# Kernel optimization log

Hardware: AMD Instinct MI355X
Metric: run time of the kernel (lower is better)

Reference implementation:

```python
import jax, jax.numpy as jnp
import numpy as np

B, Q, K, C, H = 4, 1024, 1024, 1024, 16
L = C            # latent_dim (== in_dim per module construction)
CH = L // H      # head_dim = 64


def _ln(x, w, b):
    m = jnp.mean(x, -1, keepdims=True)
    v = jnp.mean((x - m) ** 2, -1, keepdims=True)
    return (x - m) * jax.lax.rsqrt(v + 1e-5) * w + b


def setup_inputs() -> dict:
    key = jax.random.key(0)
    ks = jax.random.split(key, 16)
    s = 0.02
    return {
        "queries": jax.random.normal(ks[0], (B, Q, C), jnp.float32),
        "contexts": jax.random.normal(ks[1], (B, K, C), jnp.float32),
        "queries_hidden": jax.random.normal(ks[2], (B, Q, L), jnp.float32),
        "sa_norm_w": jnp.ones((C,), jnp.float32),
        "sa_norm_b": jnp.zeros((C,), jnp.float32),
        "sa_qkv_w": jax.random.normal(ks[3], (C, 2 * L + C), jnp.float32) * s,
        "sa_out_w": jax.random.normal(ks[4], (C, C), jnp.float32) * s,
        "sa_out_b": jnp.zeros((C,), jnp.float32),
        "ca_norm_w": jnp.ones((C,), jnp.float32),
        "ca_norm_b": jnp.zeros((C,), jnp.float32),
        "gru_w_ih": jax.random.normal(ks[5], (3 * L, C), jnp.float32) * s,
        "gru_w_hh": jax.random.normal(ks[6], (3 * L, L), jnp.float32) * s,
        "gru_b_ih": jnp.zeros((3 * L,), jnp.float32),
        "gru_b_hh": jnp.zeros((3 * L,), jnp.float32),
        "ca_k_w": jax.random.normal(ks[7], (C, L), jnp.float32) * s,
        "ca_v_w": jax.random.normal(ks[8], (C, C), jnp.float32) * s,
        "ca_out_w": jax.random.normal(ks[9], (C, C), jnp.float32) * s,
        "ca_out_b": jnp.zeros((C,), jnp.float32),
        "ln1_w": jnp.ones((C,), jnp.float32),
        "ln1_b": jnp.zeros((C,), jnp.float32),
        "lin1_w": jax.random.normal(ks[10], (C, 2 * C), jnp.float32) * s,
        "ln2_w": jnp.ones((2 * C,), jnp.float32),
        "ln2_b": jnp.zeros((2 * C,), jnp.float32),
        "lin2_w": jax.random.normal(ks[11], (2 * C, C), jnp.float32) * s,
    }


def reference(queries, contexts, queries_hidden,
              sa_norm_w, sa_norm_b, sa_qkv_w, sa_out_w, sa_out_b,
              ca_norm_w, ca_norm_b, gru_w_ih, gru_w_hh, gru_b_ih, gru_b_hh,
              ca_k_w, ca_v_w, ca_out_w, ca_out_b,
              ln1_w, ln1_b, lin1_w, ln2_w, ln2_b, lin2_w):
    scale = 1.0 / jnp.sqrt(jnp.asarray(C, queries.dtype))

    # ---- SelfAttention (pre-norm, residual) ----
    xn = _ln(queries, sa_norm_w, sa_norm_b)
    qkv = (xn @ sa_qkv_w).reshape(B, Q, H, -1)          # [B,Q,H, 2*CH + C/H]
    q, k, v = jnp.split(qkv, [CH, 2 * CH], axis=-1)
    e = jnp.einsum('nqhc,nkhc->nhqk', q, k) * scale
    a = jax.nn.softmax(e, axis=-1)
    o = jnp.einsum('nhqk,nkhc->nqhc', a, v).reshape(B, Q, C)
    x = o @ sa_out_w + sa_out_b + queries

    # ---- AttentionDynamicQuery (GRU-updated queries, cross-attn) ----
    x_pre = x
    xn = _ln(x, ca_norm_w, ca_norm_b)
    xf = xn.reshape(B * Q, C)
    hf = queries_hidden.reshape(B * Q, L)
    gi = xf @ gru_w_ih.T + gru_b_ih                     # [BQ, 3L]
    gh = hf @ gru_w_hh.T + gru_b_hh
    gir, giz, gin = jnp.split(gi, 3, axis=-1)
    ghr, ghz, ghn = jnp.split(gh, 3, axis=-1)
    r = jax.nn.sigmoid(gir + ghr)
    z = jax.nn.sigmoid(giz + ghz)
    n = jnp.tanh(gin + r * ghn)
    h = (1.0 - z) * n + z * hf                          # PyTorch GRUCell update
    qh = h.reshape(B, Q, H, CH)                         # new queries_hidden

    kk = (contexts @ ca_k_w).reshape(B, K, H, CH)
    vv = (contexts @ ca_v_w).reshape(B, K, H, C // H)
    energy = jnp.einsum('nqhc,nkhc->nhqk', qh, kk)      # returned UNscaled
    att = jax.nn.softmax(energy * scale, axis=-1)
    o = jnp.einsum('nhqk,nkhc->nqhc', att, vv).reshape(B, Q, C)
    x = o @ ca_out_w + ca_out_b + x_pre

    # ---- MLP: LN -> SiLU -> Linear -> LN -> SiLU -> Linear, residual ----
    m = jax.nn.silu(_ln(x, ln1_w, ln1_b)) @ lin1_w
    m = jax.nn.silu(_ln(m, ln2_w, ln2_b)) @ lin2_w
    out = x + m                                         # dropout(p=0) = identity
    return (out, energy, qh)
```

## Files before the change

kernel.cpp:

```cpp
#include <hip/hip_runtime.h>
#include <hip/hip_bf16.h>
#include <math.h>

static constexpr float SCALE = 0.03125f;

typedef __attribute__((ext_vector_type(4))) float f32x4;
typedef __attribute__((ext_vector_type(8))) __bf16 bf16x8;
typedef __attribute__((ext_vector_type(4))) __bf16 bf16x4;

__device__ __forceinline__ void g2l16(const void* g, void* l) {
  __builtin_amdgcn_global_load_lds(
      (const __attribute__((address_space(1))) unsigned int*)g,
      (__attribute__((address_space(3))) unsigned int*)l,
      16, 0, 0);
}

__global__ __launch_bounds__(256) void prep_all(
    const float* __restrict__ sa_qkv_w, const float* __restrict__ ca_k_w,
    const float* __restrict__ ca_v_w, const float* __restrict__ sa_out_w,
    const float* __restrict__ ca_out_w, const float* __restrict__ lin1_w,
    const float* __restrict__ lin2_w, const float* __restrict__ gru_w_ih,
    const float* __restrict__ gru_w_hh, const float* __restrict__ qhid,
    const float* __restrict__ contexts,
    __bf16* __restrict__ qkvT, __bf16* __restrict__ kT, __bf16* __restrict__ vT,
    __bf16* __restrict__ saoT, __bf16* __restrict__ caoT, __bf16* __restrict__ lin1T,
    __bf16* __restrict__ lin2T, __bf16* __restrict__ ihB, __bf16* __restrict__ hhB,
    __bf16* __restrict__ qhB, __bf16* __restrict__ ctxB) {
  int bid = blockIdx.x;
  int t = threadIdx.x;
  if (bid >= 2816) {
    const float* csrc; __bf16* cdst; int cbase;
    if (bid < 4352)      { csrc = gru_w_ih; cdst = ihB;  cbase = 2816; }
    else if (bid < 5888) { csrc = gru_w_hh; cdst = hhB;  cbase = 4352; }
    else if (bid < 7936) { csrc = qhid;     cdst = qhB;  cbase = 5888; }
    else                 { csrc = contexts; cdst = ctxB; cbase = 7936; }
    size_t idx = ((size_t)(bid - cbase) * 256 + t) * 8;
    float4 a = *(const float4*)(csrc + idx);
    float4 b = *(const float4*)(csrc + idx + 4);
    bf16x8 o = {(__bf16)a.x,(__bf16)a.y,(__bf16)a.z,(__bf16)a.w,
                (__bf16)b.x,(__bf16)b.y,(__bf16)b.z,(__bf16)b.w};
    *(bf16x8*)(cdst + idx) = o;
    return;
  }
  const float* src; __bf16* dst; int Kd, N, base;
  if (bid < 768)       { src = sa_qkv_w; dst = qkvT;  Kd = 1024; N = 3072; base = 0; }
  else if (bid < 1024) { src = ca_k_w;   dst = kT;    Kd = 1024; N = 1024; base = 768; }
  else if (bid < 1280) { src = ca_v_w;   dst = vT;    Kd = 1024; N = 1024; base = 1024; }
  else if (bid < 1536) { src = sa_out_w; dst = saoT;  Kd = 1024; N = 1024; base = 1280; }
  else if (bid < 1792) { src = ca_out_w; dst = caoT;  Kd = 1024; N = 1024; base = 1536; }
  else if (bid < 2304) { src = lin1_w;   dst = lin1T; Kd = 1024; N = 2048; base = 1792; }
  else                 { src = lin2_w;   dst = lin2T; Kd = 2048; N = 1024; base = 2304; }
  int tid = bid - base;
  int ntx = N >> 6;
  int n0 = (tid % ntx) * 64, k0 = (tid / ntx) * 64;
  __shared__ float tile[64][65];
  #pragma unroll
  for (int i = 0; i < 16; ++i) {
    int idx = i * 256 + t; int r = idx >> 6, c = idx & 63;
    tile[r][c] = src[(size_t)(k0 + r) * N + n0 + c];
  }
  __syncthreads();
  #pragma unroll
  for (int i = 0; i < 16; ++i) {
    int idx = i * 256 + t; int r = idx >> 6, c = idx & 63;
    dst[(size_t)(n0 + r) * Kd + k0 + c] = (__bf16)tile[c][r];
  }
}

template <int NV>
__global__ __launch_bounds__(256) void ln_bf16(
    const float* __restrict__ xf, const __bf16* __restrict__ xb,
    const float* __restrict__ w, const float* __restrict__ b,
    __bf16* __restrict__ out, int silu) {
  const int D = NV * 1024;
  int row = blockIdx.x, t = threadIdx.x;
  float vals[NV * 4];
  float s = 0.f, s2 = 0.f;
  #pragma unroll
  for (int i = 0; i < NV; ++i) {
    int c = (i * 256 + t) * 4;
    float4 v;
    if (xf) {
      v = *(const float4*)(xf + (size_t)row * D + c);
    } else {
      bf16x4 vb = *(const bf16x4*)(xb + (size_t)row * D + c);
      v = make_float4((float)vb[0], (float)vb[1], (float)vb[2], (float)vb[3]);
    }
    vals[i*4+0] = v.x; vals[i*4+1] = v.y; vals[i*4+2] = v.z; vals[i*4+3] = v.w;
    s += v.x + v.y + v.z + v.w;
    s2 += v.x*v.x + v.y*v.y + v.z*v.z + v.w*v.w;
  }
  #pragma unroll
  for (int off = 32; off > 0; off >>= 1) {
    s += __shfl_xor(s, off);
    s2 += __shfl_xor(s2, off);
  }
  __shared__ float red[4], red2[4];
  int wv = t >> 6;
  if ((t & 63) == 0) { red[wv] = s; red2[wv] = s2; }
  __syncthreads();
  float S  = red[0] + red[1] + red[2] + red[3];
  float S2 = red2[0] + red2[1] + red2[2] + red2[3];
  float mean = S / D;
  float var = S2 / D - mean * mean;
  float rs = rsqrtf(var + 1e-5f);
  #pragma unroll
  for (int i = 0; i < NV; ++i) {
    int c = (i * 256 + t) * 4;
    bf16x4 o;
    #pragma unroll
    for (int j = 0; j < 4; ++j) {
      float v = (vals[i*4+j] - mean) * rs * w[c+j] + b[c+j];
      if (silu) v = v / (1.f + __expf(-v));
      o[j] = (__bf16)v;
    }
    *(bf16x4*)(out + (size_t)row * D + c) = o;
  }
}

__device__ __forceinline__ void gemm_body(
    const __bf16* __restrict__ A, long long lda,
    const __bf16* __restrict__ B, long long ldb,
    float* __restrict__ outF, __bf16* __restrict__ outB, long long ldc,
    const float* __restrict__ bias, const float* __restrict__ res,
    int K, int bm, int bn) {
  __shared__ __bf16 Asm0[8192];
  __shared__ __bf16 Bsm0[8192];
  __shared__ __bf16 Asm1[8192];
  __shared__ __bf16 Bsm1[8192];
  int t = threadIdx.x;
  int lane = t & 63, w = t >> 6;
  int l15 = lane & 15, kg = lane >> 4;
  int wm = (w >> 1) * 64, wn = (w & 1) * 64;

  f32x4 acc[4][4];
  #pragma unroll
  for (int i = 0; i < 4; ++i)
    #pragma unroll
    for (int j = 0; j < 4; ++j) acc[i][j] = (f32x4)(0.0f);

  const __bf16* ga[4]; const __bf16* gb[4];
  int lo[4];
  #pragma unroll
  for (int i = 0; i < 4; ++i) {
    int slot = i * 256 + t;
    int row = slot >> 3, s = slot & 7;
    int sx = s ^ (row & 7);
    ga[i] = A + (size_t)(bm + row) * lda + (sx << 3);
    gb[i] = B + (size_t)(bn + row) * ldb + (sx << 3);
    lo[i] = (i * 256 + w * 64) << 3;
  }

  auto STAGE = [&](__bf16* As, __bf16* Bs, int k0) {
    #pragma unroll
    for (int i = 0; i < 4; ++i) g2l16(ga[i] + k0, As + lo[i]);
    #pragma unroll
    for (int i = 0; i < 4; ++i) g2l16(gb[i] + k0, Bs + lo[i]);
  };
  auto COMPUTE = [&](const __bf16* As, const __bf16* Bs) {
    #pragma unroll
    for (int kk = 0; kk < 2; ++kk) {
      bf16x8 af[4], bfr[4];
      #pragma unroll
      for (int mi = 0; mi < 4; ++mi) {
        int row = wm + mi * 16 + l15;
        int ks = kk * 4 + kg;
        af[mi] = *(const bf16x8*)(As + row * 64 + ((ks ^ (row & 7)) << 3));
      }
      #pragma unroll
      for (int ni = 0; ni < 4; ++ni) {
        int row = wn + ni * 16 + l15;
        int ks = kk * 4 + kg;
        bfr[ni] = *(const bf16x8*)(Bs + row * 64 + ((ks ^ (row & 7)) << 3));
      }
      #pragma unroll
      for (int mi = 0; mi < 4; ++mi)
        #pragma unroll
        for (int ni = 0; ni < 4; ++ni)
          acc[mi][ni] = __builtin_amdgcn_mfma_f32_16x16x32_bf16(
              af[mi], bfr[ni], acc[mi][ni], 0, 0, 0);
    }
  };
  #define GEMM_SYNC() do { \
    asm volatile("s_waitcnt vmcnt(0)" ::: "memory"); \
    __builtin_amdgcn_s_barrier(); \
    __builtin_amdgcn_sched_barrier(0); \
  } while (0)

  STAGE(Asm0, Bsm0, 0);
  GEMM_SYNC();
  int nk = K >> 6;
  for (int kt = 0; kt + 2 < nk; kt += 2) {
    STAGE(Asm1, Bsm1, (kt + 1) << 6);
    COMPUTE(Asm0, Bsm0);
    GEMM_SYNC();
    STAGE(Asm0, Bsm0, (kt + 2) << 6);
    COMPUTE(Asm1, Bsm1);
    GEMM_SYNC();
  }
  STAGE(Asm1, Bsm1, (nk - 1) << 6);
  COMPUTE(Asm0, Bsm0);
  GEMM_SYNC();
  COMPUTE(Asm1, Bsm1);
  #undef GEMM_SYNC

  #pragma unroll
  for (int mi = 0; mi < 4; ++mi) {
    #pragma unroll
    for (int ni = 0; ni < 4; ++ni) {
      int rbase = bm + wm + mi * 16 + kg * 4;
      int c = bn + wn + ni * 16 + l15;
      #pragma unroll
      for (int r = 0; r < 4; ++r) {
        float val = acc[mi][ni][r];
        if (bias) val += bias[c];
        size_t off = (size_t)(rbase + r) * ldc + c;
        if (res) val += res[off];
        if (outF) outF[off] = val;
        if (outB) outB[off] = (__bf16)val;
      }
    }
  }
}

__global__ __launch_bounds__(256) void gemm_bf16(
    const __bf16* __restrict__ A, long long lda,
    const __bf16* __restrict__ B, long long ldb,
    float* __restrict__ outF, __bf16* __restrict__ outB, long long ldc,
    const float* __restrict__ bias, const float* __restrict__ res, int K) {
  int nwg = gridDim.x * gridDim.y;
  int orig = blockIdx.y * gridDim.x + blockIdx.x;
  int swz = (orig & 7) * (nwg >> 3) + (orig >> 3);
  gemm_body(A, lda, B, ldb, outF, outB, ldc, bias, res, K,
            (swz / gridDim.x) * 128, (swz % gridDim.x) * 128);
}

__global__ __launch_bounds__(256) void gemm_dual(
    const __bf16* __restrict__ A0, long long lda0, const __bf16* __restrict__ B0, long long ldb0,
    float* __restrict__ oF0, __bf16* __restrict__ oB0, long long ldc0,
    const float* __restrict__ bias0, const float* __restrict__ res0, int K0, int gx0, int nb0,
    const __bf16* __restrict__ A1, long long lda1, const __bf16* __restrict__ B1, long long ldb1,
    float* __restrict__ oF1, __bf16* __restrict__ oB1, long long ldc1,
    const float* __restrict__ bias1, const float* __restrict__ res1, int K1, int gx1) {
  int bid = blockIdx.x;
  if (bid < nb0) {
    int swz = (bid & 7) * (nb0 >> 3) + (bid >> 3);
    gemm_body(A0, lda0, B0, ldb0, oF0, oB0, ldc0, bias0, res0, K0,
              (swz / gx0) * 128, (swz % gx0) * 128);
  } else {
    int b = bid - nb0;
    int nb1 = gridDim.x - nb0;
    int swz = (b & 7) * (nb1 >> 3) + (b >> 3);
    gemm_body(A1, lda1, B1, ldb1, oF1, oB1, ldc1, bias1, res1, K1,
              (swz / gx1) * 128, (swz % gx1) * 128);
  }
}

__global__ __launch_bounds__(256) void vtrans(
    const __bf16* __restrict__ V, long long v_sb, long long v_sh, int v_sm,
    __bf16* __restrict__ VT) {
  __shared__ __bf16 tile[64][72];
  int g = blockIdx.y, b = g >> 4, h = g & 15;
  int k0 = blockIdx.x * 64;
  const __bf16* Vb = V + (size_t)b * v_sb + (size_t)h * v_sh;
  int t = threadIdx.x;
  #pragma unroll
  for (int i = 0; i < 2; ++i) {
    int idx = i * 256 + t;
    int k = idx >> 3, dc = (idx & 7) * 8;
    bf16x8 v = *(const bf16x8*)(Vb + (size_t)(k0 + k) * v_sm + dc);
    #pragma unroll
    for (int j = 0; j < 8; ++j) tile[dc + j][k] = v[j];
  }
  __syncthreads();
  #pragma unroll
  for (int i = 0; i < 2; ++i) {
    int idx = i * 256 + t;
    int d = idx >> 3, kc = (idx & 7) * 8;
    bf16x8 v;
    #pragma unroll
    for (int j = 0; j < 8; ++j) v[j] = tile[d][kc + j];
    *(bf16x8*)(VT + ((size_t)g * 64 + d) * 1024 + k0 + kc) = v;
  }
}

template <int E>
__global__ __launch_bounds__(256) void flash_attn(
    const __bf16* __restrict__ Qb, long long q_sb, long long q_sh, int q_sm,
    const __bf16* __restrict__ Kb, long long k_sb, long long k_sh, int k_sm,
    const __bf16* __restrict__ VT, __bf16* __restrict__ Ob,
    float* __restrict__ energyOut, float scale) {
  __shared__ __bf16 Ksm[3][4096];
  __shared__ __bf16 Vsm[3][4096];
  __shared__ __bf16 Psm[128 * 64];
  __shared__ float corr_l[128];
  __shared__ float l_l[128];
  int g = blockIdx.y, b = g >> 4, h = g & 15;
  int qt = blockIdx.x * 128;
  const __bf16* Qg = Qb + (size_t)b * q_sb + (size_t)h * q_sh;
  const __bf16* Kg = Kb + (size_t)b * k_sb + (size_t)h * k_sh;
  const __bf16* Vg = VT + (size_t)g * 65536;
  int t = threadIdx.x, lane = t & 63, w = t >> 6;
  int l15 = lane & 15, kg = lane >> 4;
  int wq = w * 32;

  bf16x8 qf[2][2];
  #pragma unroll
  for (int nq = 0; nq < 2; ++nq)
    #pragma unroll
    for (int kk = 0; kk < 2; ++kk)
      qf[nq][kk] = *(const bf16x8*)(
          Qg + (size_t)(qt + wq + nq * 16 + l15) * q_sm + kk * 32 + kg * 8);

  f32x4 acc_o[2][4];
  #pragma unroll
  for (int i = 0; i < 2; ++i)
    #pragma unroll
    for (int j = 0; j < 4; ++j) acc_o[i][j] = (f32x4)(0.0f);
  float m_run[2] = {-1e30f, -1e30f};
  float l_run[2] = {0.f, 0.f};

  const __bf16* gK[2]; const __bf16* gV[2];
  int lo[2];
  #pragma unroll
  for (int i = 0; i < 2; ++i) {
    int slot = i * 256 + t;
    int row = slot >> 3, s = slot & 7, sx = s ^ (row & 7);
    gK[i] = Kg + (size_t)row * k_sm + (sx << 3);
    gV[i] = Vg + (size_t)row * 1024 + (sx << 3);
    lo[i] = (i * 256 + w * 64) << 3;
  }

  #pragma unroll
  for (int i = 0; i < 2; ++i) g2l16(gK[i], &Ksm[0][lo[i]]);
  #pragma unroll
  for (int i = 0; i < 2; ++i) g2l16(gV[i], &Vsm[0][lo[i]]);
  #pragma unroll
  for (int i = 0; i < 2; ++i) g2l16(gK[i] + (size_t)64 * k_sm, &Ksm[1][lo[i]]);
  #pragma unroll
  for (int i = 0; i < 2; ++i) g2l16(gV[i] + 64, &Vsm[1][lo[i]]);

  int rb = 0;
  for (int kvt = 0; kvt < 16; ++kvt) {
    if (E) {
      if (kvt == 0)       asm volatile("s_waitcnt vmcnt(4)" ::: "memory");
      else if (kvt == 1)  asm volatile("s_waitcnt vmcnt(12)" ::: "memory");
      else if (kvt == 15) asm volatile("s_waitcnt vmcnt(16)" ::: "memory");
      else                asm volatile("s_waitcnt vmcnt(20)" ::: "memory");
    } else {
      if (kvt == 15)      asm volatile("s_waitcnt vmcnt(0)" ::: "memory");
      else                asm volatile("s_waitcnt vmcnt(4)" ::: "memory");
    }
    __builtin_amdgcn_s_barrier();
    __builtin_amdgcn_sched_barrier(0);

    if (kvt < 14) {
      int sbuf = rb >= 1 ? rb - 1 : rb + 2;
      size_t ko = (size_t)(kvt + 2) << 6;
      #pragma unroll
      for (int i = 0; i < 2; ++i) g2l16(gK[i] + ko * k_sm, &Ksm[sbuf][lo[i]]);
      #pragma unroll
      for (int i = 0; i < 2; ++i) g2l16(gV[i] + ko, &Vsm[sbuf][lo[i]]);
    }
    const __bf16* Ks = Ksm[rb];
    const __bf16* Vs = Vsm[rb];

    f32x4 accs[4][2];
    #pragma unroll
    for (int i = 0; i < 4; ++i)
      #pragma unroll
      for (int j = 0; j < 2; ++j) accs[i][j] = (f32x4)(0.0f);
    __builtin_amdgcn_s_setprio(1);
    #pragma unroll
    for (int tt = 0; tt < 4; ++tt) {
      bf16x8 kf[2];
      #pragma unroll
      for (int kk = 0; kk < 2; ++kk) {
        int row = tt * 16 + l15;
        int ks = kk * 4 + kg;
        kf[kk] = *(const bf16x8*)(Ks + row * 64 + ((ks ^ (row & 7)) << 3));
      }
      #pragma unroll
      for (int nq = 0; nq < 2; ++nq)
        #pragma unroll
        for (int kk = 0; kk < 2; ++kk)
          accs[tt][nq] = __builtin_amdgcn_mfma_f32_16x16x32_bf16(
              kf[kk], qf[nq][kk], accs[tt][nq], 0, 0, 0);
    }
    __builtin_amdgcn_s_setprio(0);

    if (E) {
      int kv0 = kvt << 6;
      float* eg = energyOut + ((size_t)g << 20);
      #pragma unroll
      for (int nq = 0; nq < 2; ++nq) {
        int q = qt + wq + nq * 16 + l15;
        #pragma unroll
        for (int tt = 0; tt < 4; ++tt)
          __builtin_nontemporal_store(
              accs[tt][nq], (f32x4*)(eg + (size_t)q * 1024 + kv0 + tt * 16 + kg * 4));
      }
    }

    #pragma unroll
    for (int nq = 0; nq < 2; ++nq) {
      float tmax = -1e30f;
      #pragma unroll
      for (int tt = 0; tt < 4; ++tt)
        #pragma unroll
        for (int r = 0; r < 4; ++r) tmax = fmaxf(tmax, accs[tt][nq][r]);
      tmax *= scale;
      tmax = fmaxf(tmax, __shfl_xor(tmax, 16));
      tmax = fmaxf(tmax, __shfl_xor(tmax, 32));
      float m_new = fmaxf(m_run[nq], tmax);
      float corr = __expf(m_run[nq] - m_new);
      m_run[nq] = m_new;
      int q = wq + nq * 16 + l15;
      float psum = 0.f;
      #pragma unroll
      for (int tt = 0; tt < 4; ++tt) {
        bf16x4 p4;
        #pragma unroll
        for (int r = 0; r < 4; ++r) {
          float p = __expf(accs[tt][nq][r] * scale - m_new);
          psum += p;
          p4[r] = (__bf16)p;
        }
        int kvs = (tt * 16 + kg * 4) ^ ((q & 7) << 3);
        *(bf16x4*)(Psm + q * 64 + kvs) = p4;
      }
      psum += __shfl_xor(psum, 16);
      psum += __shfl_xor(psum, 32);
      l_run[nq] = l_run[nq] * corr + psum;
      if (kg == 0) corr_l[q] = corr;
    }

    #pragma unroll
    for (int mq = 0; mq < 2; ++mq) {
      f32x4 c4 = *(const f32x4*)&corr_l[wq + mq * 16 + kg * 4];
      #pragma unroll
      for (int nd = 0; nd < 4; ++nd)
        #pragma unroll
        for (int r = 0; r < 4; ++r) acc_o[mq][nd][r] *= c4[r];
    }
    __builtin_amdgcn_s_setprio(1);
    #pragma unroll
    for (int kk = 0; kk < 2; ++kk) {
      bf16x8 pf[2], vf[4];
      #pragma unroll
      for (int mq = 0; mq < 2; ++mq) {
        int row = wq + mq * 16 + l15;
        int kvs = (kk * 32 + kg * 8) ^ ((row & 7) << 3);
        pf[mq] = *(const bf16x8*)(Psm + row * 64 + kvs);
      }
      #pragma unroll
      for (int nd = 0; nd < 4; ++nd) {
        int vrow = nd * 16 + l15;
        vf[nd] = *(const bf16x8*)(Vs + vrow * 64 + (((kk * 4 + kg) ^ (vrow & 7)) << 3));
      }
      #pragma unroll
      for (int mq = 0; mq < 2; ++mq)
        #pragma unroll
        for (int nd = 0; nd < 4; ++nd)
          acc_o[mq][nd] = __builtin_amdgcn_mfma_f32_16x16x32_bf16(
              pf[mq], vf[nd], acc_o[mq][nd], 0, 0, 0);
    }
    __builtin_amdgcn_s_setprio(0);
    rb = rb == 2 ? 0 : rb + 1;
  }

  #pragma unroll
  for (int nq = 0; nq < 2; ++nq)
    if (kg == 0) l_l[wq + nq * 16 + l15] = l_run[nq];
  __syncthreads();

  #pragma unroll
  for (int mq = 0; mq < 2; ++mq) {
    f32x4 lv = *(const f32x4*)&l_l[wq + mq * 16 + kg * 4];
    #pragma unroll
    for (int nd = 0; nd < 4; ++nd) {
      int col = h * 64 + nd * 16 + l15;
      #pragma unroll
      for (int r = 0; r < 4; ++r) {
        int qrow = qt + wq + mq * 16 + kg * 4 + r;
        Ob[(size_t)(b * 1024 + qrow) * 1024 + col] = (__bf16)(acc_o[mq][nd][r] / lv[r]);
      }
    }
  }
}

__global__ __launch_bounds__(256) void gru_kernel(
    const __bf16* __restrict__ gi, const __bf16* __restrict__ gh,
    const float* __restrict__ hf, float* __restrict__ qh, __bf16* __restrict__ qhb) {
  size_t e0 = ((size_t)blockIdx.x * 256 + threadIdx.x) * 8;
  int row = (int)(e0 >> 10), col = (int)(e0 & 1023);
  size_t base = (size_t)row * 3072 + col;
  bf16x8 vir = *(const bf16x8*)(gi + base);
  bf16x8 viz = *(const bf16x8*)(gi + base + 1024);
  bf16x8 vin = *(const bf16x8*)(gi + base + 2048);
  bf16x8 vhr = *(const bf16x8*)(gh + base);
  bf16x8 vhz = *(const bf16x8*)(gh + base + 1024);
  bf16x8 vhn = *(const bf16x8*)(gh + base + 2048);
  float4 h0 = *(const float4*)(hf + e0);
  float4 h1 = *(const float4*)(hf + e0 + 4);
  float hv[8] = {h0.x, h0.y, h0.z, h0.w, h1.x, h1.y, h1.z, h1.w};
  float q[8];
  #pragma unroll
  for (int j = 0; j < 8; ++j) {
    float r = 1.f / (1.f + __expf(-((float)vir[j] + (float)vhr[j])));
    float z = 1.f / (1.f + __expf(-((float)viz[j] + (float)vhz[j])));
    float n = tanhf((float)vin[j] + r * (float)vhn[j]);
    q[j] = (1.f - z) * n + z * hv[j];
  }
  *(float4*)(qh + e0)     = make_float4(q[0], q[1], q[2], q[3]);
  *(float4*)(qh + e0 + 4) = make_float4(q[4], q[5], q[6], q[7]);
  bf16x8 qb;
  #pragma unroll
  for (int j = 0; j < 8; ++j) qb[j] = (__bf16)q[j];
  *(bf16x8*)(qhb + e0) = qb;
}

extern "C" void kernel_launch(void* const* d_in, const int* in_sizes, int n_in,
                              void* d_out, int out_size, void* d_ws, size_t ws_size,
                              hipStream_t stream) {
  (void)in_sizes; (void)n_in; (void)out_size; (void)ws_size;
  const float* queries   = (const float*)d_in[0];
  const float* contexts  = (const float*)d_in[1];
  const float* qhid      = (const float*)d_in[2];
  const float* sa_norm_w = (const float*)d_in[3];
  const float* sa_norm_b = (const float*)d_in[4];
  const float* sa_qkv_w  = (const float*)d_in[5];
  const float* sa_out_w  = (const float*)d_in[6];
  const float* sa_out_b  = (const float*)d_in[7];
  const float* ca_norm_w = (const float*)d_in[8];
  const float* ca_norm_b = (const float*)d_in[9];
  const float* gru_w_ih  = (const float*)d_in[10];
  const float* gru_w_hh  = (const float*)d_in[11];
  const float* gru_b_ih  = (const float*)d_in[12];
  const float* gru_b_hh  = (const float*)d_in[13];
  const float* ca_k_w    = (const float*)d_in[14];
  const float* ca_v_w    = (const float*)d_in[15];
  const float* ca_out_w  = (const float*)d_in[16];
  const float* ca_out_b  = (const float*)d_in[17];
  const float* ln1_w     = (const float*)d_in[18];
  const float* ln1_b     = (const float*)d_in[19];
  const float* lin1_w    = (const float*)d_in[20];
  const float* ln2_w     = (const float*)d_in[21];
  const float* ln2_b     = (const float*)d_in[22];
  const float* lin2_w    = (const float*)d_in[23];

  float* out0   = (float*)d_out;
  float* energy = out0 + (size_t)4194304;
  float* qh_out = out0 + (size_t)71303168;

  const size_t MM = 1u << 20;
  float* ws = (float*)d_ws;
  float*  X     = ws;
  float*  X2    = ws + 4 * MM;
  __bf16* M1B    = (__bf16*)(ws + 9 * MM);
  __bf16* XN_b   = (__bf16*)(ws + 17 * MM);
  __bf16* QHID_b = (__bf16*)(ws + 19 * MM);
  __bf16* CTX_b  = (__bf16*)(ws + 21 * MM);
  __bf16* O_b    = (__bf16*)(ws + 23 * MM);
  __bf16* VT_b   = (__bf16*)(ws + 25 * MM);
  __bf16* QKV_b  = (__bf16*)(ws + 27 * MM);
  __bf16* KV_b   = (__bf16*)(ws + 27 * MM);
  __bf16* LN2_b  = (__bf16*)(ws);
  __bf16* qkvT   = (__bf16*)(ws + 33 * MM);
  __bf16* ihB    = (__bf16*)(ws + 34 * MM + MM / 2);
  __bf16* hhB    = (__bf16*)(ws + 36 * MM);
  __bf16* kT     = (__bf16*)(ws + 37 * MM + MM / 2);
  __bf16* vT     = (__bf16*)(ws + 38 * MM);
  __bf16* saoT   = (__bf16*)(ws + 38 * MM + MM / 2);
  __bf16* caoT   = (__bf16*)(ws + 39 * MM);
  __bf16* lin1T  = (__bf16*)(ws + 39 * MM + MM / 2);
  __bf16* lin2T  = (__bf16*)(ws + 40 * MM + MM / 2);
  __bf16* GI_b = (__bf16*)energy;
  __bf16* GH_b = (__bf16*)(energy + 6 * MM);

  const long long QKV_SB = 1024LL * 3072;
  const long long KV_SB  = 1024LL * 2048;

  prep_all<<<9984, 256, 0, stream>>>(
      sa_qkv_w, ca_k_w, ca_v_w, sa_out_w, ca_out_w, lin1_w, lin2_w,
      gru_w_ih, gru_w_hh, qhid, contexts,
      qkvT, kT, vT, saoT, caoT, lin1T, lin2T, ihB, hhB, QHID_b, CTX_b);

  ln_bf16<1><<<4096, 256, 0, stream>>>(queries, nullptr, sa_norm_w, sa_norm_b, XN_b, 0);
  gemm_bf16<<<dim3(24, 32), 256, 0, stream>>>(
      XN_b, 1024, qkvT, 1024, nullptr, QKV_b, 3072, nullptr, nullptr, 1024);
  vtrans<<<dim3(16, 64), 256, 0, stream>>>(QKV_b + 128, QKV_SB, 192, 3072, VT_b);
  flash_attn<0><<<dim3(8, 64), 256, 0, stream>>>(
      QKV_b, QKV_SB, 192, 3072, QKV_b + 64, QKV_SB, 192, 3072,
      VT_b, O_b, nullptr, SCALE);
  gemm_dual<<<1024, 256, 0, stream>>>(
      O_b, 1024, saoT, 1024, X, nullptr, 1024, sa_out_b, queries, 1024, 8, 256,
      QHID_b, 1024, hhB, 1024, nullptr, GH_b, 3072, gru_b_hh, nullptr, 1024, 24);

  ln_bf16<1><<<4096, 256, 0, stream>>>(X, nullptr, ca_norm_w, ca_norm_b, XN_b, 0);
  gemm_dual<<<1280, 256, 0, stream>>>(
      XN_b, 1024, ihB, 1024, nullptr, GI_b, 3072, gru_b_ih, nullptr, 1024, 24, 768,
      CTX_b, 1024, kT, 1024, nullptr, KV_b, 2048, nullptr, nullptr, 1024, 16);
  gru_kernel<<<2048, 256, 0, stream>>>(GI_b, GH_b, qhid, qh_out, QHID_b );

  vtrans<<<dim3(16, 64), 256, 0, stream>>>(KV_b + 1024, KV_SB, 64, 2048, VT_b);
  flash_attn<1><<<dim3(8, 64), 256, 0, stream>>>(
      QHID_b, 1024LL * 1024, 64, 1024, KV_b, KV_SB, 64, 2048,
      VT_b, O_b, energy, SCALE);
  gemm_bf16<<<dim3(8, 32), 256, 0, stream>>>(
      O_b, 1024, caoT, 1024, X2, nullptr, 1024, ca_out_b, X, 1024);

  ln_bf16<1><<<4096, 256, 0, stream>>>(X2, nullptr, ln1_w, ln1_b, XN_b, 1);
  gemm_bf16<<<dim3(16, 32), 256, 0, stream>>>(
      XN_b, 1024, lin1T, 1024, nullptr, M1B, 2048, nullptr, nullptr, 1024);
  ln_bf16<2><<<4096, 256, 0, stream>>>(nullptr, M1B, ln2_w, ln2_b, LN2_b, 1);
  gemm_bf16<<<dim3(8, 32), 256, 0, stream>>>(
      LN2_b, 2048, lin2T, 2048, out0, nullptr, 1024, nullptr, X2, 2048);
}
```

Before: 621.7 us.

## Fuse first LayerNorm into prep and compute cross-attn V transposed directly

Folds the self-attention LayerNorm into the prep kernel as extra blocks, which removes one launch. The cross-attention V projection is now computed directly in transposed form, as vT times contexts per batch, inside the QKV gemm_dual launch. This drops the separate vtrans pass for cross-attention and shrinks the later K/V gemm to K only. It relies on vT being the transposed weight laid out so the product gives the VT layout that flash_attn expects, and on the batch offset of 1<<20 elements being correct.

```diff
diff --git a/kernel.cpp b/kernel.cpp
--- a/kernel.cpp
+++ b/kernel.cpp
@@ -22,12 +22,42 @@
     const float* __restrict__ lin2_w, const float* __restrict__ gru_w_ih,
     const float* __restrict__ gru_w_hh, const float* __restrict__ qhid,
     const float* __restrict__ contexts,
+    const float* __restrict__ queries, const float* __restrict__ sa_norm_w,
+    const float* __restrict__ sa_norm_b,
     __bf16* __restrict__ qkvT, __bf16* __restrict__ kT, __bf16* __restrict__ vT,
     __bf16* __restrict__ saoT, __bf16* __restrict__ caoT, __bf16* __restrict__ lin1T,
     __bf16* __restrict__ lin2T, __bf16* __restrict__ ihB, __bf16* __restrict__ hhB,
-    __bf16* __restrict__ qhB, __bf16* __restrict__ ctxB) {
+    __bf16* __restrict__ qhB, __bf16* __restrict__ ctxB, __bf16* __restrict__ xnB) {
   int bid = blockIdx.x;
   int t = threadIdx.x;
+  if (bid >= 9984) {
+    int row = bid - 9984;
+    int c = t * 4;
+    float4 v = *(const float4*)(queries + (size_t)row * 1024 + c);
+    float s = v.x + v.y + v.z + v.w;
+    float s2 = v.x*v.x + v.y*v.y + v.z*v.z + v.w*v.w;
+    #pragma unroll
+    for (int off = 32; off > 0; off >>= 1) {
+      s += __shfl_xor(s, off);
+      s2 += __shfl_xor(s2, off);
+    }
+    __shared__ float red[4], red2[4];
+    int wv = t >> 6;
+    if ((t & 63) == 0) { red[wv] = s; red2[wv] = s2; }
+    __syncthreads();
+    float S  = red[0] + red[1] + red[2] + red[3];
+    float S2 = red2[0] + red2[1] + red2[2] + red2[3];
+    float mean = S / 1024.f;
+    float var = S2 / 1024.f - mean * mean;
+    float rs = rsqrtf(var + 1e-5f);
+    float vv[4] = {v.x, v.y, v.z, v.w};
+    bf16x4 o;
+    #pragma unroll
+    for (int j = 0; j < 4; ++j)
+      o[j] = (__bf16)((vv[j] - mean) * rs * sa_norm_w[c+j] + sa_norm_b[c+j]);
+    *(bf16x4*)(xnB + (size_t)row * 1024 + c) = o;
+    return;
+  }
   if (bid >= 2816) {
     const float* csrc; __bf16* cdst; int cbase;
     if (bid < 4352)      { csrc = gru_w_ih; cdst = ihB;  cbase = 2816; }
@@ -241,7 +271,8 @@
     const float* __restrict__ bias0, const float* __restrict__ res0, int K0, int gx0, int nb0,
     const __bf16* __restrict__ A1, long long lda1, const __bf16* __restrict__ B1, long long ldb1,
     float* __restrict__ oF1, __bf16* __restrict__ oB1, long long ldc1,
-    const float* __restrict__ bias1, const float* __restrict__ res1, int K1, int gx1) {
+    const float* __restrict__ bias1, const float* __restrict__ res1, int K1, int gx1,
+    int batchB1) {
   int bid = blockIdx.x;
   if (bid < nb0) {
     int swz = (bid & 7) * (nb0 >> 3) + (bid >> 3);
@@ -251,8 +282,16 @@
     int b = bid - nb0;
     int nb1 = gridDim.x - nb0;
     int swz = (b & 7) * (nb1 >> 3) + (b >> 3);
-    gemm_body(A1, lda1, B1, ldb1, oF1, oB1, ldc1, bias1, res1, K1,
-              (swz / gx1) * 128, (swz % gx1) * 128);
+    int tm = swz / gx1, bn = (swz % gx1) * 128;
+    if (batchB1) {
+      int batch = tm >> 3;
+      gemm_body(A1, lda1, B1 + ((size_t)batch << 20), ldb1, nullptr,
+                oB1 + ((size_t)batch << 20), ldc1, bias1, res1, K1,
+                (tm & 7) * 128, bn);
+    } else {
+      gemm_body(A1, lda1, B1, ldb1, oF1, oB1, ldc1, bias1, res1, K1,
+                tm * 128, bn);
+    }
   }
 }
 
@@ -558,13 +597,14 @@
   float*  X     = ws;
   float*  X2    = ws + 4 * MM;
   __bf16* M1B    = (__bf16*)(ws + 9 * MM);
+  __bf16* VT_CA  = (__bf16*)(ws + 13 * MM);
   __bf16* XN_b   = (__bf16*)(ws + 17 * MM);
   __bf16* QHID_b = (__bf16*)(ws + 19 * MM);
   __bf16* CTX_b  = (__bf16*)(ws + 21 * MM);
   __bf16* O_b    = (__bf16*)(ws + 23 * MM);
-  __bf16* VT_b   = (__bf16*)(ws + 25 * MM);
+  __bf16* VT_SA  = (__bf16*)(ws + 25 * MM);
   __bf16* QKV_b  = (__bf16*)(ws + 27 * MM);
-  __bf16* KV_b   = (__bf16*)(ws + 27 * MM);
+  __bf16* K_b    = (__bf16*)(ws + 27 * MM);
   __bf16* LN2_b  = (__bf16*)(ws);
   __bf16* qkvT   = (__bf16*)(ws + 33 * MM);
   __bf16* ihB    = (__bf16*)(ws + 34 * MM + MM / 2);
@@ -579,34 +619,32 @@
   __bf16* GH_b = (__bf16*)(energy + 6 * MM);
 
   const long long QKV_SB = 1024LL * 3072;
-  const long long KV_SB  = 1024LL * 2048;
-
-  prep_all<<<9984, 256, 0, stream>>>(
+
+  prep_all<<<14080, 256, 0, stream>>>(
       sa_qkv_w, ca_k_w, ca_v_w, sa_out_w, ca_out_w, lin1_w, lin2_w,
-      gru_w_ih, gru_w_hh, qhid, contexts,
-      qkvT, kT, vT, saoT, caoT, lin1T, lin2T, ihB, hhB, QHID_b, CTX_b);
-
-  ln_bf16<1><<<4096, 256, 0, stream>>>(queries, nullptr, sa_norm_w, sa_norm_b, XN_b, 0);
-  gemm_bf16<<<dim3(24, 32), 256, 0, stream>>>(
-      XN_b, 1024, qkvT, 1024, nullptr, QKV_b, 3072, nullptr, nullptr, 1024);
-  vtrans<<<dim3(16, 64), 256, 0, stream>>>(QKV_b + 128, QKV_SB, 192, 3072, VT_b);
+      gru_w_ih, gru_w_hh, qhid, contexts, queries, sa_norm_w, sa_norm_b,
+      qkvT, kT, vT, saoT, caoT, lin1T, lin2T, ihB, hhB, QHID_b, CTX_b, XN_b);
+
+  gemm_dual<<<1024, 256, 0, stream>>>(
+      XN_b, 1024, qkvT, 1024, nullptr, QKV_b, 3072, nullptr, nullptr, 1024, 24, 768,
+      vT, 1024, CTX_b, 1024, nullptr, VT_CA, 1024, nullptr, nullptr, 1024, 8, 1);
+  vtrans<<<dim3(16, 64), 256, 0, stream>>>(QKV_b + 128, QKV_SB, 192, 3072, VT_SA);
   flash_attn<0><<<dim3(8, 64), 256, 0, stream>>>(
       QKV_b, QKV_SB, 192, 3072, QKV_b + 64, QKV_SB, 192, 3072,
-      VT_b, O_b, nullptr, SCALE);
+      VT_SA, O_b, nullptr, SCALE);
   gemm_dual<<<1024, 256, 0, stream>>>(
       O_b, 1024, saoT, 1024, X, nullptr, 1024, sa_out_b, queries, 1024, 8, 256,
-      QHID_b, 1024, hhB, 1024, nullptr, GH_b, 3072, gru_b_hh, nullptr, 1024, 24);
+      QHID_b, 1024, hhB, 1024, nullptr, GH_b, 3072, gru_b_hh, nullptr, 1024, 24, 0);
 
   ln_bf16<1><<<4096, 256, 0, stream>>>(X, nullptr, ca_norm_w, ca_norm_b, XN_b, 0);
-  gemm_dual<<<1280, 256, 0, stream>>>(
+  gemm_dual<<<1024, 256, 0, stream>>>(
       XN_b, 1024, ihB, 1024, nullptr, GI_b, 3072, gru_b_ih, nullptr, 1024, 24, 768,
-      CTX_b, 1024, kT, 1024, nullptr, KV_b, 2048, nullptr, nullptr, 1024, 16);
+      CTX_b, 1024, kT, 1024, nullptr, K_b, 1024, nullptr, nullptr, 1024, 8, 0);
   gru_kernel<<<2048, 256, 0, stream>>>(GI_b, GH_b, qhid, qh_out, QHID_b );
 
-  vtrans<<<dim3(16, 64), 256, 0, stream>>>(KV_b + 1024, KV_SB, 64, 2048, VT_b);
   flash_attn<1><<<dim3(8, 64), 256, 0, stream>>>(
-      QHID_b, 1024LL * 1024, 64, 1024, KV_b, KV_SB, 64, 2048,
-      VT_b, O_b, energy, SCALE);
+      QHID_b, 1024LL * 1024, 64, 1024, K_b, 1024LL * 1024, 64, 1024,
+      VT_CA, O_b, energy, SCALE);
   gemm_bf16<<<dim3(8, 32), 256, 0, stream>>>(
       O_b, 1024, caoT, 1024, X2, nullptr, 1024, ca_out_b, X, 1024);
 
```

Result: slower. 640.7 us (+3.1%).
